# Kernel optimization log

Measured on AMD Instinct MI355X. Metric: run time of the kernel, lower is better.

## Reference

```python
import jax, jax.numpy as jnp
import numpy as np

B, N, D, H, NW = 16, 400, 256, 8, 4
DH = D // H
EPS_LN = 1e-5

def _layer_norm(x, g, b):
    m = jnp.mean(x, axis=-1, keepdims=True)
    v = jnp.mean((x - m) ** 2, axis=-1, keepdims=True)
    return (x - m) / jnp.sqrt(v + EPS_LN) * g + b

def setup_inputs() -> dict:
    key = jax.random.key(0)
    ks = jax.random.split(key, 10)
    p = lambda k, shape: (jax.random.normal(k, shape, jnp.float32) * 0.02)
    return {
        'x': jax.random.normal(ks[0], (B, N, D), jnp.float32),
        'attention_weights': jax.random.normal(ks[1], (B, NW, N, N), jnp.float32),
        'Wq': p(ks[2], (D, D)), 'bq': jnp.zeros((D,), jnp.float32),
        'Wk': p(ks[3], (D, D)), 'bk': jnp.zeros((D,), jnp.float32),
        'Wv': p(ks[4], (D, D)), 'bv': jnp.zeros((D,), jnp.float32),
        'Wo': p(ks[5], (D, D)), 'bo': jnp.zeros((D,), jnp.float32),
        'g1': jnp.ones((D,), jnp.float32), 'beta1': jnp.zeros((D,), jnp.float32),
        'W1': p(ks[6], (4 * D, D)), 'b1': jnp.zeros((4 * D,), jnp.float32),
        'W2': p(ks[7], (D, 4 * D)), 'b2': jnp.zeros((D,), jnp.float32),
        'g2': jnp.ones((D,), jnp.float32), 'beta2': jnp.zeros((D,), jnp.float32),
    }

def reference(x, attention_weights, Wq, bq, Wk, bk, Wv, bv, Wo, bo,
              g1, beta1, W1, b1, W2, b2, g2, beta2):
    b, n, d = x.shape
    # QKV projections, split heads: [B, H, N, DH]
    q = (x @ Wq.T + bq).reshape(b, n, H, DH).transpose(0, 2, 1, 3)
    k = (x @ Wk.T + bk).reshape(b, n, H, DH).transpose(0, 2, 1, 3)
    v = (x @ Wv.T + bv).reshape(b, n, H, DH).transpose(0, 2, 1, 3)
    qk = jnp.einsum('bhnd,bhmd->bhnm', q, k) / np.sqrt(DH)  # [B,H,N,N]
    # signed attention averaged over the NW per-sample weight matrices
    nw = attention_weights.shape[1]
    scores = jnp.zeros_like(qk)
    for i in range(nw):  # small fixed count, not a data dim
        w = attention_weights[:, i][:, None, :, :]  # [B,1,N,N]
        s = qk * w
        e = jnp.exp(jnp.abs(s))
        scores = scores + jnp.sign(s) * e / (jnp.sum(e, axis=-1, keepdims=True) + 1e-10)
    scores = scores / nw
    attn_out = jnp.einsum('bhnm,bhmd->bhnd', scores, v)
    attn_out = attn_out.transpose(0, 2, 1, 3).reshape(b, n, d)
    attn_out = attn_out @ Wo.T + bo
    h = _layer_norm(x + attn_out, g1, beta1)
    ffn = jax.nn.relu(h @ W1.T + b1) @ W2.T + b2
    y = _layer_norm(h + ffn, g2, beta2)
    return (y, scores)
```

## Files before the change

### kernel.cpp

```cpp
#include <hip/hip_runtime.h>
#include <hip/hip_fp16.h>

typedef unsigned int uint32;

#define B_ 16
#define N_ 400
#define D_ 256
#define H_ 8
#define DH_ 32
#define NW_ 4

#if __has_builtin(__builtin_amdgcn_exp2f)
#define EXP2(x) __builtin_amdgcn_exp2f(x)
#else
#define EXP2(x) exp2f(x)
#endif

#define QK_SCL 0.2550348f

using bf16x8 = __attribute__((ext_vector_type(8))) short;
using f16x8  = __attribute__((ext_vector_type(8))) _Float16;
using f16x4  = __attribute__((ext_vector_type(4))) _Float16;
using f32x4  = __attribute__((ext_vector_type(4))) float;

__device__ __forceinline__ ushort f2b(float f) {
  uint32 u = __float_as_uint(f);
  uint32 r = (u + 0x7fffu + ((u >> 16) & 1u)) >> 16;
  return (ushort)r;
}

__global__ __launch_bounds__(256) void convert_kernel(
    const float* __restrict__ x,  const float* __restrict__ wq,
    const float* __restrict__ wk, const float* __restrict__ wv,
    const float* __restrict__ wo, const float* __restrict__ w1,
    const float* __restrict__ w2,
    ushort* __restrict__ xb,  ushort* __restrict__ wqb,
    ushort* __restrict__ wkb, ushort* __restrict__ wvb,
    ushort* __restrict__ wob, ushort* __restrict__ w1b,
    ushort* __restrict__ w2b) {
  int gid = blockIdx.x * 256 + threadIdx.x;
  const float* src; ushort* dst;
  if      (gid < 409600) { src = x;  dst = xb;  }
  else if ((gid -= 409600) < 16384) { src = wq; dst = wqb; }
  else if ((gid -= 16384) < 16384)  { src = wk; dst = wkb; }
  else if ((gid -= 16384) < 16384)  { src = wv; dst = wvb; }
  else if ((gid -= 16384) < 16384)  { src = wo; dst = wob; }
  else if ((gid -= 16384) < 65536)  { src = w1; dst = w1b; }
  else { gid -= 65536; src = w2; dst = w2b; }
  float4 f = ((const float4*)src)[gid];
  ushort4 u;
  u.x = f2b(f.x); u.y = f2b(f.y); u.z = f2b(f.z); u.w = f2b(f.w);
  *(ushort4*)&dst[(size_t)gid * 4] = u;
}

template <int RELU, int RESID, int OUT_F32, int OUT_BF16>
__global__ __launch_bounds__(256) void gemm_bt(
    const ushort* __restrict__ A, const ushort* __restrict__ W,
    const float* __restrict__ bias, const float* __restrict__ resid,
    float* __restrict__ outf, ushort* __restrict__ outb,
    int M, int N, int K) {
  __shared__ __align__(16) ushort As[2][64 * 40];
  __shared__ __align__(16) ushort Ws[2][64 * 40];
  int t = threadIdx.x;
  int l = t & 63, w = t >> 6;
  int n0 = blockIdx.x * 64, m0 = blockIdx.y * 64;
  int srow = t >> 2, sc = (t & 3) * 8;
  int lrow = l & 15, lk = (l >> 4) * 8;

  const uint4* ag = (const uint4*)&A[(size_t)(m0 + srow) * K + sc];
  const uint4* wg = (const uint4*)&W[(size_t)(n0 + srow) * K + sc];
  uint4 ar = ag[0], wr = wg[0];
  int nk = K >> 5;

  f32x4 acc[4];
#pragma unroll
  for (int nt = 0; nt < 4; nt++) acc[nt] = {0.f, 0.f, 0.f, 0.f};

  for (int kk = 0; kk < nk; kk++) {
    int cur = kk & 1;
    *(uint4*)&As[cur][srow * 40 + sc] = ar;
    *(uint4*)&Ws[cur][srow * 40 + sc] = wr;
    if (kk + 1 < nk) { ar = ag[(size_t)(kk + 1) * 4]; wr = wg[(size_t)(kk + 1) * 4]; }
    __syncthreads();
    bf16x8 af = *(const bf16x8*)&As[cur][(16 * w + lrow) * 40 + lk];
#pragma unroll
    for (int nt = 0; nt < 4; nt++) {
      bf16x8 bf = *(const bf16x8*)&Ws[cur][(nt * 16 + lrow) * 40 + lk];
      acc[nt] = __builtin_amdgcn_mfma_f32_16x16x32_bf16(af, bf, acc[nt], 0, 0, 0);
    }
  }

#pragma unroll
  for (int nt = 0; nt < 4; nt++) {
    int n = n0 + nt * 16 + lrow;
    float bv = bias[n];
#pragma unroll
    for (int r = 0; r < 4; r++) {
      int m = m0 + 16 * w + (l >> 4) * 4 + r;
      float v = acc[nt][r] + bv;
      if (RELU)  v = fmaxf(v, 0.f);
      if (RESID) v += resid[(size_t)m * N + n];
      if (OUT_F32)  outf[(size_t)m * N + n] = v;
      if (OUT_BF16) outb[(size_t)m * N + n] = f2b(v);
    }
  }
}

__global__ __launch_bounds__(256) void qkv_gemm(
    const ushort* __restrict__ xb, const ushort* __restrict__ wq,
    const ushort* __restrict__ wk, const ushort* __restrict__ wv,
    const float* __restrict__ bq, const float* __restrict__ bk,
    const float* __restrict__ bv,
    _Float16* __restrict__ qh, _Float16* __restrict__ kh,
    _Float16* __restrict__ vt) {
  __shared__ __align__(16) ushort As[2][64 * 40];
  __shared__ __align__(16) ushort Ws[2][64 * 40];
  int z = blockIdx.z;
  const ushort* W = (z == 0) ? wq : (z == 1) ? wk : wv;
  const float* bias = (z == 0) ? bq : (z == 1) ? bk : bv;

  int t = threadIdx.x;
  int l = t & 63, w = t >> 6;
  int n0 = blockIdx.x * 64, m0 = blockIdx.y * 64;
  int srow = t >> 2, sc = (t & 3) * 8;
  int lrow = l & 15, lk = (l >> 4) * 8;

  const uint4* ag = (const uint4*)&xb[(size_t)(m0 + srow) * 256 + sc];
  const uint4* wg = (const uint4*)&W[(size_t)(n0 + srow) * 256 + sc];
  uint4 ar = ag[0], wr = wg[0];

  f32x4 acc[4];
#pragma unroll
  for (int nt = 0; nt < 4; nt++) acc[nt] = {0.f, 0.f, 0.f, 0.f};

  for (int kk = 0; kk < 8; kk++) {
    int cur = kk & 1;
    *(uint4*)&As[cur][srow * 40 + sc] = ar;
    *(uint4*)&Ws[cur][srow * 40 + sc] = wr;
    if (kk + 1 < 8) { ar = ag[(kk + 1) * 4]; wr = wg[(kk + 1) * 4]; }
    __syncthreads();
    bf16x8 af = *(const bf16x8*)&As[cur][(16 * w + lrow) * 40 + lk];
#pragma unroll
    for (int nt = 0; nt < 4; nt++) {
      bf16x8 bf = *(const bf16x8*)&Ws[cur][(nt * 16 + lrow) * 40 + lk];
      acc[nt] = __builtin_amdgcn_mfma_f32_16x16x32_bf16(af, bf, acc[nt], 0, 0, 0);
    }
  }

  int mb = m0 + 16 * w + (l >> 4) * 4;
  int bb = mb / 400;
  int mi = mb - bb * 400;
#pragma unroll
  for (int nt = 0; nt < 4; nt++) {
    int n = n0 + nt * 16 + lrow;
    float bvv = bias[n];
    if (z < 2) {
      _Float16* out = z ? kh : qh;
      float scl = z ? 1.f : QK_SCL;
      int hh = n >> 5, dd = n & 31;
      _Float16* dst = out + (((size_t)(bb * 8 + hh)) * 400 + mi) * 32 + dd;
#pragma unroll
      for (int r = 0; r < 4; r++)
        dst[(size_t)r * 32] = (_Float16)((acc[nt][r] + bvv) * scl);
    } else {
      _Float16 h4[4];
#pragma unroll
      for (int r = 0; r < 4; r++) h4[r] = (_Float16)(acc[nt][r] + bvv);
      *(uint2*)&vt[((size_t)bb * 256 + n) * 400 + mi] = *(uint2*)h4;
    }
  }
}

#define SP 416

__global__ __launch_bounds__(256, 4) void attn_kernel(
    const _Float16* __restrict__ qh, const _Float16* __restrict__ kh,
    const _Float16* __restrict__ vt, const float* __restrict__ aw,
    float* __restrict__ scores, ushort* __restrict__ attnb) {
  __shared__ __align__(16) char smem[16 * SP * 2];
  __half* S = (__half*)smem;

  int id = blockIdx.x;
  int c = ((id >> 6) << 3) | (id & 7);
  int hh = (id >> 3) & 7;
  int b = c / 25;
  int n0 = (c - b * 25) * 16;

  int t = threadIdx.x;
  int w = t >> 6, l = t & 63;
  int lq = l >> 4, lr = l & 15;

  {
    const _Float16* qbase = qh + (((size_t)(b * 8 + hh)) * 400 + n0) * 32;
    const _Float16* kbase = kh + ((size_t)(b * 8 + hh)) * 400 * 32;
    f16x8 af = *(const f16x8*)(qbase + lr * 32 + lq * 8);
    for (int mt = w; mt < 25; mt += 4) {
      f16x8 bf = *(const f16x8*)(kbase + (size_t)(mt * 16 + lr) * 32 + lq * 8);
      f32x4 cc = {0.f, 0.f, 0.f, 0.f};
      cc = __builtin_amdgcn_mfma_f32_16x16x32_f16(af, bf, cc, 0, 0, 0);
#pragma unroll
      for (int r = 0; r < 4; r++)
        S[(lq * 4 + r) * SP + mt * 16 + lr] = __float2half(cc[r]);
    }
  }
  __syncthreads();

  {
    int m0 = l * 4, m1 = 256 + l * 4;
    bool act = (l < 36);
    int m1c = act ? m1 : m0;
    const float* awb = aw + (((size_t)(b * 4)) * 400 + n0) * 400;
    float* scb = scores + (((size_t)(b * 8 + hh)) * 400 + n0) * 400;

    float4 A0[4], A1[4], B0[4], B1[4];
    {
      const float* awn = awb + (size_t)w * 400;
#pragma unroll
      for (int i = 0; i < 4; i++) {
        A0[i] = *(const float4*)(awn + (size_t)i * 160000 + m0);
        A1[i] = *(const float4*)(awn + (size_t)i * 160000 + m1c);
      }
    }

    auto grp = [&](int n, float4 (&c0)[4], float4 (&c1)[4],
                   float4 (&p0)[4], float4 (&p1)[4], bool pf) {
      if (pf) {
        const float* awn = awb + (size_t)(n + 4) * 400;
#pragma unroll
        for (int i = 0; i < 4; i++) {
          p0[i] = *(const float4*)(awn + (size_t)i * 160000 + m0);
          p1[i] = *(const float4*)(awn + (size_t)i * 160000 + m1c);
        }
      }
      _Float16* srow = (_Float16*)S + (size_t)n * SP;
      float* scout = scb + (size_t)n * 400;

      f16x4 s0 = *(const f16x4*)(srow + m0);
      float q0[4], q1[4];
#pragma unroll
      for (int j = 0; j < 4; j++) q0[j] = (float)s0[j];
      if (act) {
        f16x4 s1 = *(const f16x4*)(srow + m1);
#pragma unroll
        for (int j = 0; j < 4; j++) q1[j] = (float)s1[j];
      } else {
#pragma unroll
        for (int j = 0; j < 4; j++) q1[j] = 0.f;
      }

      f16x4 e0[4], e1[4];
      float z[4];
#pragma unroll
      for (int i = 0; i < 4; i++) {
        float zz0 = 0.f, zz1 = 0.f;
#pragma unroll
        for (int j = 0; j < 4; j++) {
          float tt = q0[j] * ((const float*)&c0[i])[j];
          float ef = EXP2(fabsf(tt));
          zz0 += ef;
          e0[i][j] = (_Float16)copysignf(ef, tt);
        }
#pragma unroll
        for (int j = 0; j < 4; j++) {
          float tt = q1[j] * ((const float*)&c1[i])[j];
          float ef = EXP2(fabsf(tt));
          zz1 += ef;
          e1[i][j] = (_Float16)copysignf(ef, tt);
        }
        z[i] = zz0 + (act ? zz1 : 0.f);
      }

#pragma unroll
      for (int o = 1; o <= 32; o <<= 1) {
#pragma unroll
        for (int i = 0; i < 4; i++) z[i] += __shfl_xor(z[i], o);
      }

      f16x4 o0, o1;
#pragma unroll
      for (int j = 0; j < 4; j++) { o0[j] = (_Float16)0.f; o1[j] = (_Float16)0.f; }
#pragma unroll
      for (int i = 0; i < 4; i++) {
        _Float16 zh = (_Float16)(0.25f / (z[i] + 1e-10f));
        f16x4 zv = {zh, zh, zh, zh};
        o0 += e0[i] * zv;
        o1 += e1[i] * zv;
      }

      float4 so;
#pragma unroll
      for (int j = 0; j < 4; j++) ((float*)&so)[j] = (float)o0[j];
      *(float4*)(scout + m0) = so;
      *(f16x4*)(srow + m0) = o0;
      if (act) {
        float4 s1o;
#pragma unroll
        for (int j = 0; j < 4; j++) ((float*)&s1o)[j] = (float)o1[j];
        *(float4*)(scout + m1) = s1o;
        *(f16x4*)(srow + m1) = o1;
      } else if (l < 40) {
        f16x4 hz;
#pragma unroll
        for (int j = 0; j < 4; j++) hz[j] = (_Float16)0.f;
        *(f16x4*)(srow + m1) = hz;
      }
    };

    grp(w,      A0, A1, B0, B1, true);
    grp(4 + w,  B0, B1, A0, A1, true);
    grp(8 + w,  A0, A1, B0, B1, true);
    grp(12 + w, B0, B1, A0, A1, false);
  }
  __syncthreads();

  const _Float16* vbase = vt + (((size_t)b) * 256 + hh * 32) * 400;
  f32x4 a0 = {0.f, 0.f, 0.f, 0.f}, a1 = {0.f, 0.f, 0.f, 0.f};
  const _Float16* Sh = (const _Float16*)S;
  for (int c2 = w; c2 < 13; c2 += 4) {
    f16x8 sf = *(const f16x8*)(Sh + lr * SP + c2 * 32 + lq * 8);
    f16x8 v0 = *(const f16x8*)(vbase + (size_t)lr * 400 + c2 * 32 + lq * 8);
    f16x8 v1 = *(const f16x8*)(vbase + (size_t)(16 + lr) * 400 + c2 * 32 + lq * 8);
    a0 = __builtin_amdgcn_mfma_f32_16x16x32_f16(sf, v0, a0, 0, 0, 0);
    a1 = __builtin_amdgcn_mfma_f32_16x16x32_f16(sf, v1, a1, 0, 0, 0);
  }
  __syncthreads();
  float* Of = (float*)smem;
#pragma unroll
  for (int r = 0; r < 4; r++) {
    Of[(w * 16 + lq * 4 + r) * 32 + lr] = a0[r];
    Of[(w * 16 + lq * 4 + r) * 32 + 16 + lr] = a1[r];
  }
  __syncthreads();
  for (int o = t; o < 512; o += 256) {
    int n = o >> 5, d = o & 31;
    float s = Of[n * 32 + d] + Of[512 + n * 32 + d] +
              Of[1024 + n * 32 + d] + Of[1536 + n * 32 + d];
    attnb[((size_t)(b * 400 + n0 + n)) * 256 + hh * 32 + d] = f2b(s);
  }
}

__global__ __launch_bounds__(256) void ln_kernel(
    const float* __restrict__ src, const float* __restrict__ g,
    const float* __restrict__ be, float* __restrict__ outf,
    ushort* __restrict__ outb) {
  int row = blockIdx.x, t = threadIdx.x;
  float v = src[(size_t)row * 256 + t];
  __shared__ float red[4];
  float s = v;
#pragma unroll
  for (int o = 32; o > 0; o >>= 1) s += __shfl_down(s, o, 64);
  if ((t & 63) == 0) red[t >> 6] = s;
  __syncthreads();
  float mean = (red[0] + red[1] + red[2] + red[3]) * (1.f / 256.f);
  __syncthreads();
  float d = v - mean;
  s = d * d;
#pragma unroll
  for (int o = 32; o > 0; o >>= 1) s += __shfl_down(s, o, 64);
  if ((t & 63) == 0) red[t >> 6] = s;
  __syncthreads();
  float var = (red[0] + red[1] + red[2] + red[3]) * (1.f / 256.f);
  float y = d * rsqrtf(var + 1e-5f) * g[t] + be[t];
  outf[(size_t)row * 256 + t] = y;
  if (outb) outb[(size_t)row * 256 + t] = f2b(y);
}

extern "C" void kernel_launch(void* const* d_in, const int* in_sizes, int n_in,
                              void* d_out, int out_size, void* d_ws,
                              size_t ws_size, hipStream_t stream) {
  const float* x   = (const float*)d_in[0];
  const float* aw  = (const float*)d_in[1];
  const float* Wq  = (const float*)d_in[2];
  const float* bq  = (const float*)d_in[3];
  const float* Wk  = (const float*)d_in[4];
  const float* bk  = (const float*)d_in[5];
  const float* Wv  = (const float*)d_in[6];
  const float* bv  = (const float*)d_in[7];
  const float* Wo  = (const float*)d_in[8];
  const float* bo  = (const float*)d_in[9];
  const float* g1  = (const float*)d_in[10];
  const float* be1 = (const float*)d_in[11];
  const float* W1  = (const float*)d_in[12];
  const float* b1  = (const float*)d_in[13];
  const float* W2  = (const float*)d_in[14];
  const float* b2  = (const float*)d_in[15];
  const float* g2  = (const float*)d_in[16];
  const float* be2 = (const float*)d_in[17];

  if (ws_size < 34340864) return;

  char* ws = (char*)d_ws;
  ushort*   xb    = (ushort*)(ws + 0);
  ushort*   wqb   = (ushort*)(ws + 3276800);
  ushort*   wkb   = (ushort*)(ws + 3407872);
  ushort*   wvb   = (ushort*)(ws + 3538944);
  ushort*   wob   = (ushort*)(ws + 3670016);
  ushort*   w1b   = (ushort*)(ws + 3801088);
  ushort*   w2b   = (ushort*)(ws + 4325376);
  _Float16* qhb   = (_Float16*)(ws + 4849664);
  _Float16* khb   = (_Float16*)(ws + 8126464);
  _Float16* vtb   = (_Float16*)(ws + 11403264);
  ushort*   attnb = (ushort*)(ws + 14680064);
  float*    ao    = (float*)(ws + 17956864);
  float*    hbuf  = (float*)(ws + 24510464);
  ushort*   hb    = (ushort*)(ws + 31064064);
  ushort*   ffn1b = (ushort*)qhb;
  float*    ffn2  = ao;

  float* yout   = (float*)d_out;
  float* scores = yout + 1638400;

  convert_kernel<<<2368, 256, 0, stream>>>(x, Wq, Wk, Wv, Wo, W1, W2,
                                           xb, wqb, wkb, wvb, wob, w1b, w2b);
  qkv_gemm<<<dim3(4, 100, 3), 256, 0, stream>>>(
      xb, wqb, wkb, wvb, bq, bk, bv, qhb, khb, vtb);
  attn_kernel<<<3200, 256, 0, stream>>>(qhb, khb, vtb, aw, scores, attnb);
  gemm_bt<0, 1, 1, 0><<<dim3(4, 100), 256, 0, stream>>>(
      attnb, wob, bo, x, ao, nullptr, 6400, 256, 256);
  ln_kernel<<<6400, 256, 0, stream>>>(ao, g1, be1, hbuf, hb);
  gemm_bt<1, 0, 0, 1><<<dim3(16, 100), 256, 0, stream>>>(
      hb, w1b, b1, nullptr, nullptr, ffn1b, 6400, 1024, 256);
  gemm_bt<0, 1, 1, 0><<<dim3(4, 100), 256, 0, stream>>>(
      ffn1b, w2b, b2, hbuf, ffn2, nullptr, 6400, 256, 1024);
  ln_kernel<<<6400, 256, 0, stream>>>(ffn2, g2, be2, yout, nullptr);
}
```

Before: 250.4 us.

## Fuse output-projection and FFN2 GEMMs with residual add and LayerNorm

Adds a gemm_ln kernel where each block computes 32 full rows of 256 output columns, then applies bias, residual, and a one-pass LayerNorm (sum and sum-of-squares) in registers. It replaces two GEMM + ln_kernel pairs, which removes the fp32 intermediate round trips through global memory and two launches. The cost is a grid of only 200 blocks, which may underfill the GPU compared with the previous 400-block GEMMs, and variance computed as E[x^2]-mean^2, which is less numerically stable.

```diff
diff --git a/kernel.cpp b/kernel.cpp
--- a/kernel.cpp
+++ b/kernel.cpp
@@ -106,6 +106,133 @@
   }
 }
 
+template <int OUT_BF16>
+__global__ __launch_bounds__(256) void gemm_ln(
+    const ushort* __restrict__ A, const ushort* __restrict__ W,
+    const float* __restrict__ bias, const float* __restrict__ resid,
+    const float* __restrict__ g, const float* __restrict__ be,
+    float* __restrict__ outf, ushort* __restrict__ outb, int K) {
+  __shared__ __align__(16) ushort As[2][32 * 40];
+  __shared__ __align__(16) ushort Ws[2][256 * 40];
+  __shared__ float2 red[4][32];
+  int t = threadIdx.x;
+  int l = t & 63, w = t >> 6;
+  int m0 = blockIdx.x * 32;
+  int lrow = l & 15, lk = (l >> 4) * 8;
+  int srow = t >> 2, sc = (t & 3) * 8;
+  int nk = K >> 5;
+
+  const uint4* ag  = (const uint4*)&A[(size_t)(m0 + srow) * K + sc];
+  const uint4* wg0 = (const uint4*)&W[(size_t)(srow) * K + sc];
+  const uint4* wg1 = (const uint4*)&W[(size_t)(64 + srow) * K + sc];
+  const uint4* wg2 = (const uint4*)&W[(size_t)(128 + srow) * K + sc];
+  const uint4* wg3 = (const uint4*)&W[(size_t)(192 + srow) * K + sc];
+
+  uint4 ar = {0, 0, 0, 0};
+  if (t < 128) ar = ag[0];
+  uint4 w0 = wg0[0], w1 = wg1[0], w2 = wg2[0], w3 = wg3[0];
+
+  f32x4 acc[2][4];
+#pragma unroll
+  for (int fr = 0; fr < 2; fr++)
+#pragma unroll
+    for (int fc = 0; fc < 4; fc++) acc[fr][fc] = {0.f, 0.f, 0.f, 0.f};
+
+  for (int kk = 0; kk < nk; kk++) {
+    int cur = kk & 1;
+    if (t < 128) *(uint4*)&As[cur][srow * 40 + sc] = ar;
+    *(uint4*)&Ws[cur][srow * 40 + sc]         = w0;
+    *(uint4*)&Ws[cur][(64 + srow) * 40 + sc]  = w1;
+    *(uint4*)&Ws[cur][(128 + srow) * 40 + sc] = w2;
+    *(uint4*)&Ws[cur][(192 + srow) * 40 + sc] = w3;
+    if (kk + 1 < nk) {
+      size_t off = (size_t)(kk + 1) * 4;
+      if (t < 128) ar = ag[off];
+      w0 = wg0[off]; w1 = wg1[off]; w2 = wg2[off]; w3 = wg3[off];
+    }
+    __syncthreads();
+    bf16x8 af[2], bf[4];
+#pragma unroll
+    for (int fr = 0; fr < 2; fr++)
+      af[fr] = *(const bf16x8*)&As[cur][(fr * 16 + lrow) * 40 + lk];
+#pragma unroll
+    for (int fc = 0; fc < 4; fc++)
+      bf[fc] = *(const bf16x8*)&Ws[cur][(w * 64 + fc * 16 + lrow) * 40 + lk];
+#pragma unroll
+    for (int fr = 0; fr < 2; fr++)
+#pragma unroll
+      for (int fc = 0; fc < 4; fc++)
+        acc[fr][fc] = __builtin_amdgcn_mfma_f32_16x16x32_bf16(
+            af[fr], bf[fc], acc[fr][fc], 0, 0, 0);
+  }
+
+  float s[2][4], ss[2][4];
+#pragma unroll
+  for (int fr = 0; fr < 2; fr++)
+#pragma unroll
+    for (int r = 0; r < 4; r++) { s[fr][r] = 0.f; ss[fr][r] = 0.f; }
+
+#pragma unroll
+  for (int fr = 0; fr < 2; fr++) {
+#pragma unroll
+    for (int fc = 0; fc < 4; fc++) {
+      int n = w * 64 + fc * 16 + lrow;
+      float bv = bias[n];
+#pragma unroll
+      for (int r = 0; r < 4; r++) {
+        int m = m0 + fr * 16 + (l >> 4) * 4 + r;
+        float v = acc[fr][fc][r] + bv + resid[(size_t)m * 256 + n];
+        acc[fr][fc][r] = v;
+        s[fr][r] += v;
+        ss[fr][r] += v * v;
+      }
+    }
+  }
+#pragma unroll
+  for (int o = 1; o <= 8; o <<= 1) {
+#pragma unroll
+    for (int fr = 0; fr < 2; fr++)
+#pragma unroll
+      for (int r = 0; r < 4; r++) {
+        s[fr][r] += __shfl_xor(s[fr][r], o);
+        ss[fr][r] += __shfl_xor(ss[fr][r], o);
+      }
+  }
+  if (lrow == 0) {
+#pragma unroll
+    for (int fr = 0; fr < 2; fr++)
+#pragma unroll
+      for (int r = 0; r < 4; r++) {
+        int row = fr * 16 + (l >> 4) * 4 + r;
+        red[w][row] = {s[fr][r], ss[fr][r]};
+      }
+  }
+  __syncthreads();
+
+#pragma unroll
+  for (int fr = 0; fr < 2; fr++) {
+#pragma unroll
+    for (int r = 0; r < 4; r++) {
+      int row = fr * 16 + (l >> 4) * 4 + r;
+      float2 p0 = red[0][row], p1 = red[1][row];
+      float2 p2 = red[2][row], p3 = red[3][row];
+      float sum = p0.x + p1.x + p2.x + p3.x;
+      float sq  = p0.y + p1.y + p2.y + p3.y;
+      float mean = sum * (1.f / 256.f);
+      float var = sq * (1.f / 256.f) - mean * mean;
+      float rinv = rsqrtf(var + 1e-5f);
+      int m = m0 + row;
+#pragma unroll
+      for (int fc = 0; fc < 4; fc++) {
+        int n = w * 64 + fc * 16 + lrow;
+        float y = (acc[fr][fc][r] - mean) * rinv * g[n] + be[n];
+        outf[(size_t)m * 256 + n] = y;
+        if (OUT_BF16) outb[(size_t)m * 256 + n] = f2b(y);
+      }
+    }
+  }
+}
+
 __global__ __launch_bounds__(256) void qkv_gemm(
     const ushort* __restrict__ xb, const ushort* __restrict__ wq,
     const ushort* __restrict__ wk, const ushort* __restrict__ wv,
@@ -337,32 +464,6 @@
               Of[1024 + n * 32 + d] + Of[1536 + n * 32 + d];
     attnb[((size_t)(b * 400 + n0 + n)) * 256 + hh * 32 + d] = f2b(s);
   }
-}
-
-__global__ __launch_bounds__(256) void ln_kernel(
-    const float* __restrict__ src, const float* __restrict__ g,
-    const float* __restrict__ be, float* __restrict__ outf,
-    ushort* __restrict__ outb) {
-  int row = blockIdx.x, t = threadIdx.x;
-  float v = src[(size_t)row * 256 + t];
-  __shared__ float red[4];
-  float s = v;
-#pragma unroll
-  for (int o = 32; o > 0; o >>= 1) s += __shfl_down(s, o, 64);
-  if ((t & 63) == 0) red[t >> 6] = s;
-  __syncthreads();
-  float mean = (red[0] + red[1] + red[2] + red[3]) * (1.f / 256.f);
-  __syncthreads();
-  float d = v - mean;
-  s = d * d;
-#pragma unroll
-  for (int o = 32; o > 0; o >>= 1) s += __shfl_down(s, o, 64);
-  if ((t & 63) == 0) red[t >> 6] = s;
-  __syncthreads();
-  float var = (red[0] + red[1] + red[2] + red[3]) * (1.f / 256.f);
-  float y = d * rsqrtf(var + 1e-5f) * g[t] + be[t];
-  outf[(size_t)row * 256 + t] = y;
-  if (outb) outb[(size_t)row * 256 + t] = f2b(y);
 }
 
 extern "C" void kernel_launch(void* const* d_in, const int* in_sizes, int n_in,
@@ -405,7 +506,7 @@
   float*    hbuf  = (float*)(ws + 24510464);
   ushort*   hb    = (ushort*)(ws + 31064064);
   ushort*   ffn1b = (ushort*)qhb;
-  float*    ffn2  = ao;
+  (void)ao;
 
   float* yout   = (float*)d_out;
   float* scores = yout + 1638400;
@@ -415,12 +516,10 @@
   qkv_gemm<<<dim3(4, 100, 3), 256, 0, stream>>>(
       xb, wqb, wkb, wvb, bq, bk, bv, qhb, khb, vtb);
   attn_kernel<<<3200, 256, 0, stream>>>(qhb, khb, vtb, aw, scores, attnb);
-  gemm_bt<0, 1, 1, 0><<<dim3(4, 100), 256, 0, stream>>>(
-      attnb, wob, bo, x, ao, nullptr, 6400, 256, 256);
-  ln_kernel<<<6400, 256, 0, stream>>>(ao, g1, be1, hbuf, hb);
+  gemm_ln<1><<<200, 256, 0, stream>>>(attnb, wob, bo, x, g1, be1,
+                                      hbuf, hb, 256);
   gemm_bt<1, 0, 0, 1><<<dim3(16, 100), 256, 0, stream>>>(
       hb, w1b, b1, nullptr, nullptr, ffn1b, 6400, 1024, 256);
-  gemm_bt<0, 1, 1, 0><<<dim3(4, 100), 256, 0, stream>>>(
-      ffn1b, w2b, b2, hbuf, ffn2, nullptr, 6400, 256, 1024);
-  ln_kernel<<<6400, 256, 0, stream>>>(ffn2, g2, be2, yout, nullptr);
-}
+  gemm_ln<0><<<200, 256, 0, stream>>>(ffn1b, w2b, b2, hbuf, g2, be2,
+                                      yout, nullptr, 1024);
+}
```

Result: faster. 241.8 us (-3.4%).
